# Optimization experiments

Hardware: AMD Instinct MI355X
Metric: run time of the kernel (lower is better)

## Reference

```python
import jax, jax.numpy as jnp
import numpy as np

N = 8192
NFEAT = 512
NHID = 512
NCLASS = 8
EPS = 1e-9
ADJ_P = 0.01  # edge density


def setup_inputs() -> dict:
    key = jax.random.key(0)
    ks = jax.random.split(key, 16)
    adj = (jax.random.uniform(ks[0], (N, N)) < ADJ_P).astype(jnp.float32)
    x = jax.random.normal(ks[1], (N, NFEAT), dtype=jnp.float32)
    s_in = 1.0 / np.sqrt(NFEAT)
    s_h = 1.0 / np.sqrt(NHID)
    return {
        "adj": adj,
        "x": x,
        "gcn1_W": jax.random.normal(ks[2], (NFEAT, NHID), jnp.float32) * s_in,
        "gcn1_b": jnp.zeros((NHID,), jnp.float32),
        "Qw": jax.random.normal(ks[3], (NHID, NHID), jnp.float32) * s_h,
        "Qb": jnp.zeros((NHID,), jnp.float32),
        "Kw": jax.random.normal(ks[4], (NHID, NHID), jnp.float32) * s_h,
        "Kb": jnp.zeros((NHID,), jnp.float32),
        "Vw": jax.random.normal(ks[5], (NHID, NHID), jnp.float32) * s_h,
        "Vb": jnp.zeros((NHID,), jnp.float32),
        "ln_g": jnp.ones((NHID,), jnp.float32),
        "ln_b": jnp.zeros((NHID,), jnp.float32),
        "gcn2_W": jax.random.normal(ks[6], (NHID, NCLASS), jnp.float32) * s_h,
        "gcn2_b": jnp.zeros((NCLASS,), jnp.float32),
    }


def _gcn_norm(a):
    # symmetric degree normalization D^{-1/2} A D^{-1/2}, degrees = row sums
    d_inv_sqrt = jax.lax.rsqrt(a.sum(axis=1) + EPS)  # [N]
    return d_inv_sqrt[:, None] * a * d_inv_sqrt[None, :]


def _layer_norm(x, g, b):
    mu = x.mean(axis=-1, keepdims=True)
    var = x.var(axis=-1, keepdims=True)
    return (x - mu) * jax.lax.rsqrt(var + 1e-5) * g + b


def reference(adj, x, gcn1_W, gcn1_b, Qw, Qb, Kw, Kb, Vw, Vb, ln_g, ln_b, gcn2_W, gcn2_b):
    # GraphConvolution: adj @ (x W) + b, then ReLU
    h = jax.nn.relu(adj @ (x @ gcn1_W) + gcn1_b)  # [N, NHID]
    Qh = h @ Qw + Qb
    Kh = h @ Kw + Kb
    Vh = h @ Vw + Vb
    # adjacency-masked dense scores (multiplicative mask, as in original)
    A_tilde = adj * (Qh @ Kh.T)  # [N, N]
    attention = jax.nn.softmax(A_tilde, axis=1)
    X_tilde = _gcn_norm(attention) @ Vh  # [N, NHID]
    X_tilde = _layer_norm(X_tilde, ln_g, ln_b)
    z = adj @ (X_tilde @ gcn2_W) + gcn2_b  # [N, NCLASS]
    return jax.nn.softmax(z, axis=1)
```

## Files before the change

kernel.cpp:

```cpp
#include <hip/hip_runtime.h>
#include <math.h>

#define N_NODES 8192
#define NFEAT 512
#define NHID 512
#define NCLASS 8
#define RCAP 192
#define KB_SPLIT 1536
#define KA_SPLIT 1024
#define CANDCAP 64
#define FILTER_MARGIN 96.0f
#define SROWS 4

#define PB_SPLITA 256
#define PB_SPLITB (PB_SPLITA + 4096)
#define PB_SPLITV (PB_SPLITB + 768)
#define PB_BIAS   (PB_SPLITV + 768)
#define PB_MISC   (PB_BIAS + 129)
#define PB_TOTAL  (PB_MISC + 6)

__device__ inline ushort f2bf(float f) {
  uint32_t u = __float_as_uint(f);
  uint32_t r = u + 0x7fffu + ((u >> 16) & 1u);
  return (ushort)(r >> 16);
}
__device__ inline float bf2f(ushort h) { return __uint_as_float(((uint32_t)h) << 16); }

__global__ __launch_bounds__(256) void build_ell(const float* __restrict__ adj,
                                                 int* __restrict__ colidx,
                                                 int* __restrict__ deg) {
  int row = blockIdx.x;
  __shared__ int cnt;
  __shared__ int cols[RCAP];
  if (threadIdx.x == 0) cnt = 0;
  __syncthreads();
  const float4* arow = (const float4*)(adj + (size_t)row * N_NODES);
#pragma unroll
  for (int it = 0; it < N_NODES / 4 / 256; ++it) {
    int i = it * 256 + threadIdx.x;
    float4 v = arow[i];
    int base = i * 4;
    if (v.x > 0.5f) { int p = atomicAdd(&cnt, 1); if (p < RCAP) cols[p] = base; }
    if (v.y > 0.5f) { int p = atomicAdd(&cnt, 1); if (p < RCAP) cols[p] = base + 1; }
    if (v.z > 0.5f) { int p = atomicAdd(&cnt, 1); if (p < RCAP) cols[p] = base + 2; }
    if (v.w > 0.5f) { int p = atomicAdd(&cnt, 1); if (p < RCAP) cols[p] = base + 3; }
    __syncthreads();
  }
  int d = cnt < RCAP ? cnt : RCAP;
  if (threadIdx.x == 0) deg[row] = d;
  for (int i = threadIdx.x; i < d; i += 256) colidx[(size_t)row * RCAP + i] = cols[i];
}

__global__ __launch_bounds__(256) void prep_all(
    const float* __restrict__ Kw, float* __restrict__ KwT,
    const float* __restrict__ x, ushort* __restrict__ Xs,
    const float* __restrict__ W1, ushort* __restrict__ W1ts,
    const float* __restrict__ Vw, ushort* __restrict__ Bcts,
    const float* __restrict__ Qw, const float* __restrict__ Qb, const float* __restrict__ Kb,
    float* __restrict__ u, float* __restrict__ w, float* __restrict__ cbuf,
    const float* __restrict__ Vb, float* __restrict__ bcat, float* __restrict__ T) {
  __shared__ float tile[32][33];
  int b = blockIdx.x, t = threadIdx.x;
  if (b < PB_SPLITA) {
    int bx = b & 15, by = b >> 4;
    int tx = t & 31, ty = t >> 5;
    int xcol = bx * 32 + tx, y0 = by * 32;
    for (int i = ty; i < 32; i += 8) tile[i][tx] = Kw[(size_t)(y0 + i) * 512 + xcol];
    __syncthreads();
    int xo = by * 32 + tx, yo0 = bx * 32;
    for (int i = ty; i < 32; i += 8) KwT[(size_t)(yo0 + i) * 512 + xo] = tile[tx][i];
  } else if (b < PB_SPLITB) {
    int idx = (b - PB_SPLITA) * 256 + t;
    int m = idx >> 7, tc = idx & 127;
    float4 v = ((const float4*)(x + (size_t)m * 512))[tc];
    ushort4 hi, lo;
    hi.x = f2bf(v.x); hi.y = f2bf(v.y); hi.z = f2bf(v.z); hi.w = f2bf(v.w);
    lo.x = f2bf(v.x - bf2f(hi.x)); lo.y = f2bf(v.y - bf2f(hi.y));
    lo.z = f2bf(v.z - bf2f(hi.z)); lo.w = f2bf(v.w - bf2f(hi.w));
    ushort* row = Xs + (size_t)m * KA_SPLIT;
    ((ushort4*)row)[tc] = hi;
    ((ushort4*)(row + 512))[tc] = lo;
  } else if (b < PB_SPLITV) {
    int idx = (b - PB_SPLITB) * 256 + t;
    int n = idx / 384, tc = idx % 384;
    int sec = tc >> 7;
    int k0 = (tc & 127) << 2;
    ushort4 o;
    float f0 = W1[(size_t)(k0 + 0) * 512 + n];
    float f1 = W1[(size_t)(k0 + 1) * 512 + n];
    float f2 = W1[(size_t)(k0 + 2) * 512 + n];
    float f3 = W1[(size_t)(k0 + 3) * 512 + n];
    if (sec == 1) {
      o.x = f2bf(f0 - bf2f(f2bf(f0))); o.y = f2bf(f1 - bf2f(f2bf(f1)));
      o.z = f2bf(f2 - bf2f(f2bf(f2))); o.w = f2bf(f3 - bf2f(f2bf(f3)));
    } else {
      o.x = f2bf(f0); o.y = f2bf(f1); o.z = f2bf(f2); o.w = f2bf(f3);
    }
    ((ushort4*)(W1ts + (size_t)n * KB_SPLIT))[tc] = o;
  } else if (b < PB_BIAS) {
    int idx = (b - PB_SPLITV) * 256 + t;
    int n = idx / 384, tc = idx % 384;
    const float* src = Vw + n;
    int sec = tc >> 7;
    int k0 = (tc & 127) << 2;
    ushort4 o;
    float f0 = src[(size_t)(k0 + 0) * 512];
    float f1 = src[(size_t)(k0 + 1) * 512];
    float f2 = src[(size_t)(k0 + 2) * 512];
    float f3 = src[(size_t)(k0 + 3) * 512];
    if (sec == 1) {
      o.x = f2bf(f0 - bf2f(f2bf(f0))); o.y = f2bf(f1 - bf2f(f2bf(f1)));
      o.z = f2bf(f2 - bf2f(f2bf(f2))); o.w = f2bf(f3 - bf2f(f2bf(f3)));
    } else {
      o.x = f2bf(f0); o.y = f2bf(f1); o.z = f2bf(f2); o.w = f2bf(f3);
    }
    ((ushort4*)(Bcts + (size_t)(512 + n) * KB_SPLIT))[tc] = o;
  } else if (b < PB_MISC) {
    int k = (b - PB_BIAS) * 4 + (t >> 6);
    int lane = t & 63;
    if (k > NHID) return;
    if (k == NHID) {
      float s = 0.f;
      for (int j = lane; j < NHID; j += 64) s = fmaf(Qb[j], Kb[j], s);
#pragma unroll
      for (int o = 32; o > 0; o >>= 1) s += __shfl_down(s, o, 64);
      if (lane == 0) cbuf[0] = s;
      return;
    }
    float su = 0.f, sw = 0.f;
    for (int j = lane; j < NHID; j += 64) {
      su = fmaf(Qw[(size_t)k * NHID + j], Kb[j], su);
      sw = fmaf(Kw[(size_t)k * NHID + j], Qb[j], sw);
    }
#pragma unroll
    for (int o = 32; o > 0; o >>= 1) { su += __shfl_down(su, o, 64); sw += __shfl_down(sw, o, 64); }
    if (lane == 0) { u[k] = su; w[k] = sw; }
  } else {
    int i = (b - PB_MISC) * 256 + t;
    if (i < 1024) bcat[i] = (i < 512) ? 0.f : Vb[i - 512];
    else if (i < 1536) T[i - 1024] = 0.f;
  }
}

__global__ __launch_bounds__(256) void split_mmat(const float* __restrict__ Mm, ushort* __restrict__ Bt) {
  int idx = blockIdx.x * 256 + threadIdx.x;
  int n = idx / 384, tc = idx % 384;
  const float* src = Mm + n;
  int sec = tc >> 7;
  int k0 = (tc & 127) << 2;
  ushort4 o;
  float f0 = src[(size_t)(k0 + 0) * 512];
  float f1 = src[(size_t)(k0 + 1) * 512];
  float f2 = src[(size_t)(k0 + 2) * 512];
  float f3 = src[(size_t)(k0 + 3) * 512];
  if (sec == 1) {
    o.x = f2bf(f0 - bf2f(f2bf(f0))); o.y = f2bf(f1 - bf2f(f2bf(f1)));
    o.z = f2bf(f2 - bf2f(f2bf(f2))); o.w = f2bf(f3 - bf2f(f2bf(f3)));
  } else {
    o.x = f2bf(f0); o.y = f2bf(f1); o.z = f2bf(f2); o.w = f2bf(f3);
  }
  ((ushort4*)(Bt + (size_t)n * KB_SPLIT))[tc] = o;
}

__global__ __launch_bounds__(256) void sgemm64x128(const float* __restrict__ A,
                                                   const float* __restrict__ B,
                                                   float* __restrict__ C,
                                                   int M, int Nn, int K, int ldc) {
  __shared__ float As[16][68];
  __shared__ float Bs[16][132];
  const int tid = threadIdx.x;
  const int bm = blockIdx.y * 64, bn = blockIdx.x * 128;
  const int tx = tid & 15, ty = tid >> 4;
  const int arow = tid >> 2, acol = (tid & 3) << 2;
  const int brow = tid >> 4, bcol = (tid & 15) << 2;
  float acc[4][8];
#pragma unroll
  for (int i = 0; i < 4; ++i)
#pragma unroll
    for (int j = 0; j < 8; ++j) acc[i][j] = 0.f;
  const float* Ap = A + (size_t)(bm + arow) * K + acol;
  const float* Bp = B + (size_t)brow * Nn + bn + bcol;
  float4 av = *(const float4*)(Ap);
  float4 bv0 = *(const float4*)(Bp);
  float4 bv1 = *(const float4*)(Bp + 64);
  for (int k0 = 0; k0 < K; k0 += 16) {
    if (k0) __syncthreads();
    As[acol + 0][arow] = av.x;
    As[acol + 1][arow] = av.y;
    As[acol + 2][arow] = av.z;
    As[acol + 3][arow] = av.w;
    *(float4*)&Bs[brow][bcol] = bv0;
    *(float4*)&Bs[brow][bcol + 64] = bv1;
    __syncthreads();
    int kn = (k0 + 16 < K) ? k0 + 16 : 0;
    av = *(const float4*)(Ap + kn);
    bv0 = *(const float4*)(Bp + (size_t)kn * Nn);
    bv1 = *(const float4*)(Bp + (size_t)kn * Nn + 64);
#pragma unroll
    for (int kk = 0; kk < 16; ++kk) {
      float4 a = *(const float4*)&As[kk][ty << 2];
      float4 b0 = *(const float4*)&Bs[kk][tx << 2];
      float4 b1 = *(const float4*)&Bs[kk][(tx << 2) + 64];
      float ar[4] = {a.x, a.y, a.z, a.w};
      float br[8] = {b0.x, b0.y, b0.z, b0.w, b1.x, b1.y, b1.z, b1.w};
#pragma unroll
      for (int i = 0; i < 4; ++i)
#pragma unroll
        for (int j = 0; j < 8; ++j) acc[i][j] = fmaf(ar[i], br[j], acc[i][j]);
    }
  }
#pragma unroll
  for (int i = 0; i < 4; ++i) {
    int r = bm + (ty << 2) + i;
    *(float4*)(C + (size_t)r * ldc + bn + (tx << 2)) =
        make_float4(acc[i][0], acc[i][1], acc[i][2], acc[i][3]);
    *(float4*)(C + (size_t)r * ldc + bn + 64 + (tx << 2)) =
        make_float4(acc[i][4], acc[i][5], acc[i][6], acc[i][7]);
  }
}

using frag_ab = __attribute__((ext_vector_type(8))) short;
using frag_cd = __attribute__((ext_vector_type(4))) float;

__global__ __launch_bounds__(256) void mfma_gemm_bt(const ushort* __restrict__ A,
                                                    const ushort* __restrict__ Bt,
                                                    const float* __restrict__ bias,
                                                    float* __restrict__ C,
                                                    int ldc, float* __restrict__ Tsum) {
  __shared__ __align__(16) ushort Atile[128 * 64];
  __shared__ __align__(16) ushort Btile[128 * 64];
  const int tid = threadIdx.x;
  const int w = tid >> 6, lane = tid & 63;
  const int m0 = blockIdx.y * 128, n0 = blockIdx.x * 128;
  const int wm = (w >> 1) * 64, wn = (w & 1) * 64;
  const int q = lane >> 4, c16 = lane & 15;

  frag_cd acc[4][4];
#pragma unroll
  for (int i = 0; i < 4; ++i)
#pragma unroll
    for (int j = 0; j < 4; ++j) acc[i][j] = (frag_cd){0.f, 0.f, 0.f, 0.f};

  const int srow = (w << 3) + (lane >> 3);
  const int scolb = (lane & 7) << 4;
  const uint8_t* gA = (const uint8_t*)A + (size_t)(m0 + srow) * (KA_SPLIT * 2) + scolb;
  const uint8_t* gB = (const uint8_t*)Bt + (size_t)(n0 + srow) * (KB_SPLIT * 2) + scolb;

  for (int c = 0; c < 24; ++c) {
    const size_t kaB = (size_t)((c < 8 ? c : c - 8) * 128);
    const size_t kbB = (size_t)(c * 128);
#pragma unroll
    for (int r = 0; r < 4; ++r) {
      __builtin_amdgcn_global_load_lds(
          (const __attribute__((address_space(1))) uint32_t*)(gA + (size_t)(r * 32) * (KA_SPLIT * 2) + kaB),
          (__attribute__((address_space(3))) uint32_t*)((uint8_t*)Atile + r * 4096 + w * 1024), 16, 0, 0);
      __builtin_amdgcn_global_load_lds(
          (const __attribute__((address_space(1))) uint32_t*)(gB + (size_t)(r * 32) * (KB_SPLIT * 2) + kbB),
          (__attribute__((address_space(3))) uint32_t*)((uint8_t*)Btile + r * 4096 + w * 1024), 16, 0, 0);
    }
    __syncthreads();
#pragma unroll
    for (int kk = 0; kk < 2; ++kk) {
      frag_ab af[4], bf[4];
#pragma unroll
      for (int i = 0; i < 4; ++i) {
        af[i] = *(const frag_ab*)((const uint8_t*)Atile + (wm + i * 16 + c16) * 128 + kk * 64 + q * 16);
        bf[i] = *(const frag_ab*)((const uint8_t*)Btile + (wn + i * 16 + c16) * 128 + kk * 64 + q * 16);
      }
#pragma unroll
      for (int i = 0; i < 4; ++i)
#pragma unroll
        for (int j = 0; j < 4; ++j)
          acc[i][j] = __builtin_amdgcn_mfma_f32_16x16x32_bf16(af[i], bf[j], acc[i][j], 0, 0, 0);
    }
    __syncthreads();
  }
#pragma unroll
  for (int j = 0; j < 4; ++j) {
    int col = n0 + wn + j * 16 + c16;
    float bv = bias ? bias[col] : 0.f;
    float csum = 0.f;
#pragma unroll
    for (int i = 0; i < 4; ++i) {
      int row = m0 + wm + i * 16 + q * 4;
#pragma unroll
      for (int r = 0; r < 4; ++r) {
        float v = acc[i][j][r] + bv;
        C[(size_t)(row + r) * ldc + col] = v;
        csum += v;
      }
    }
    if (Tsum && col >= 512) {
      csum += __shfl_xor(csum, 16, 64);
      csum += __shfl_xor(csum, 32, 64);
      if (q == 0) atomicAdd(&Tsum[col - 512], csum);
    }
  }
}

__global__ __launch_bounds__(256, 8) void spmm_persist(const float* __restrict__ xW,
                                                       const int* __restrict__ colidx,
                                                       const int* __restrict__ deg,
                                                       const float* __restrict__ b1,
                                                       const float* __restrict__ u, const float* __restrict__ w,
                                                       float* __restrict__ h, ushort* __restrict__ Hs,
                                                       float* __restrict__ a_vec, float* __restrict__ b_vec) {
  __shared__ int scols[SROWS][RCAP];
  __shared__ float4 part[128];
  __shared__ float ra[2], rb[2];
  int t = threadIdx.x, half = t >> 7, tt = t & 127;
  int row0 = blockIdx.x * SROWS;
  int d[SROWS];
#pragma unroll
  for (int r = 0; r < SROWS; ++r) {
    d[r] = deg[row0 + r];
    for (int i = t; i < d[r]; i += 256) scols[r][i] = colidx[(size_t)(row0 + r) * RCAP + i];
  }
  __syncthreads();
#pragma unroll 1
  for (int r = 0; r < SROWS; ++r) {
    int row = row0 + r, dd = d[r];
    float4 acc = make_float4(0.f, 0.f, 0.f, 0.f);
    int e = half;
    for (; e + 14 < dd; e += 16) {
      float4 v0 = ((const float4*)(xW + (size_t)scols[r][e + 0] * NHID))[tt];
      float4 v1 = ((const float4*)(xW + (size_t)scols[r][e + 2] * NHID))[tt];
      float4 v2 = ((const float4*)(xW + (size_t)scols[r][e + 4] * NHID))[tt];
      float4 v3 = ((const float4*)(xW + (size_t)scols[r][e + 6] * NHID))[tt];
      float4 v4 = ((const float4*)(xW + (size_t)scols[r][e + 8] * NHID))[tt];
      float4 v5 = ((const float4*)(xW + (size_t)scols[r][e + 10] * NHID))[tt];
      float4 v6 = ((const float4*)(xW + (size_t)scols[r][e + 12] * NHID))[tt];
      float4 v7 = ((const float4*)(xW + (size_t)scols[r][e + 14] * NHID))[tt];
      acc.x += ((v0.x + v1.x) + (v2.x + v3.x)) + ((v4.x + v5.x) + (v6.x + v7.x));
      acc.y += ((v0.y + v1.y) + (v2.y + v3.y)) + ((v4.y + v5.y) + (v6.y + v7.y));
      acc.z += ((v0.z + v1.z) + (v2.z + v3.z)) + ((v4.z + v5.z) + (v6.z + v7.z));
      acc.w += ((v0.w + v1.w) + (v2.w + v3.w)) + ((v4.w + v5.w) + (v6.w + v7.w));
    }
    for (; e < dd; e += 2) {
      float4 v = ((const float4*)(xW + (size_t)scols[r][e] * NHID))[tt];
      acc.x += v.x; acc.y += v.y; acc.z += v.z; acc.w += v.w;
    }
    if (half == 1) part[tt] = acc;
    __syncthreads();
    if (half == 0) {
      float4 p = part[tt];
      acc.x += p.x; acc.y += p.y; acc.z += p.z; acc.w += p.w;
      float4 bv = ((const float4*)b1)[tt];
      float4 o = make_float4(fmaxf(acc.x + bv.x, 0.f), fmaxf(acc.y + bv.y, 0.f),
                             fmaxf(acc.z + bv.z, 0.f), fmaxf(acc.w + bv.w, 0.f));
      ((float4*)(h + (size_t)row * NHID))[tt] = o;
      ushort4 hi, lo;
      hi.x = f2bf(o.x); hi.y = f2bf(o.y); hi.z = f2bf(o.z); hi.w = f2bf(o.w);
      lo.x = f2bf(o.x - bf2f(hi.x)); lo.y = f2bf(o.y - bf2f(hi.y));
      lo.z = f2bf(o.z - bf2f(hi.z)); lo.w = f2bf(o.w - bf2f(hi.w));
      ushort* hr = Hs + (size_t)row * KA_SPLIT;
      ((ushort4*)hr)[tt] = hi;
      ((ushort4*)(hr + 512))[tt] = lo;
      float4 uv = ((const float4*)u)[tt], wv4 = ((const float4*)w)[tt];
      float sa = fmaf(o.x, uv.x, fmaf(o.y, uv.y, fmaf(o.z, uv.z, o.w * uv.w)));
      float sb = fmaf(o.x, wv4.x, fmaf(o.y, wv4.y, fmaf(o.z, wv4.z, o.w * wv4.w)));
      int wid = tt >> 6, lane = tt & 63;
#pragma unroll
      for (int off = 32; off > 0; off >>= 1) { sa += __shfl_down(sa, off, 64); sb += __shfl_down(sb, off, 64); }
      if (lane == 0) { ra[wid] = sa; rb[wid] = sb; }
    }
    __syncthreads();
    if (t == 0) { a_vec[row] = ra[0] + ra[1]; b_vec[row] = rb[0] + rb[1]; }
    __syncthreads();
  }
}

__global__ __launch_bounds__(256) void score2_agg_ln(
    const float* __restrict__ G, int ldg, const float* __restrict__ h,
    const ushort* __restrict__ Hs, const int* __restrict__ colidx, const int* __restrict__ deg,
    const float* __restrict__ a_vec, const float* __restrict__ b_vec,
    const float* __restrict__ cbuf, const float* __restrict__ Vh, int ldv,
    const float* __restrict__ T, const float* __restrict__ lng,
    const float* __restrict__ lnb, const float* __restrict__ W2, float* __restrict__ Y) {
  __shared__ int scols[4][RCAP];
  __shared__ float sbv[4][RCAP];
  __shared__ float sv[4][RCAP];
  __shared__ int cand[4][CANDCAP];
  __shared__ int ccnt[4];
  __shared__ float w2s[NHID * NCLASS];
  int t = threadIdx.x, wv = t >> 6, lane = t & 63;
  int row = blockIdx.x * 4 + wv;
  int d = deg[row];
  int q = lane >> 4, u = lane & 15;
  for (int i = t; i < NHID * NCLASS; i += 256) w2s[i] = W2[i];
  if (lane == 0) ccnt[wv] = 0;
  float4 ga4[4][2];
  const float4* Gr4 = (const float4*)(G + (size_t)row * ldg);
#pragma unroll
  for (int it2 = 0; it2 < 4; ++it2) {
    ga4[it2][0] = Gr4[it2 * 32 + 2 * u];
    ga4[it2][1] = Gr4[it2 * 32 + 2 * u + 1];
  }
  for (int i = lane; i < d; i += 64) {
    int c = colidx[(size_t)row * RCAP + i];
    scols[wv][i] = c;
    sbv[wv][i] = b_vec[c];
  }
  __syncthreads();
  for (int e0 = 0; e0 < d; e0 += 4) {
    int e = e0 + q;
    bool act = e < d;
    int col = scols[wv][act ? e : 0];
    const uint4* hr = (const uint4*)(Hs + (size_t)col * KA_SPLIT);
    float s_a = 0.f, s_b = 0.f;
#pragma unroll
    for (int it2 = 0; it2 < 4; ++it2) {
      uint4 p = hr[it2 * 16 + u];
      float4 g0 = ga4[it2][0], g1 = ga4[it2][1];
      s_a = fmaf(__uint_as_float(p.x << 16), g0.x, s_a);
      s_a = fmaf(__uint_as_float(p.x & 0xffff0000u), g0.y, s_a);
      s_a = fmaf(__uint_as_float(p.y << 16), g0.z, s_a);
      s_a = fmaf(__uint_as_float(p.y & 0xffff0000u), g0.w, s_a);
      s_b = fmaf(__uint_as_float(p.z << 16), g1.x, s_b);
      s_b = fmaf(__uint_as_float(p.z & 0xffff0000u), g1.y, s_b);
      s_b = fmaf(__uint_as_float(p.w << 16), g1.z, s_b);
      s_b = fmaf(__uint_as_float(p.w & 0xffff0000u), g1.w, s_b);
    }
    float s = s_a + s_b;
    s += __shfl_down(s, 8, 16);
    s += __shfl_down(s, 4, 16);
    s += __shfl_down(s, 2, 16);
    s += __shfl_down(s, 1, 16);
    if (u == 0 && act) sv[wv][e] = s + sbv[wv][e];
  }
  __syncthreads();
  float fm = -1e30f;
  for (int i = lane; i < d; i += 64) fm = fmaxf(fm, sv[wv][i]);
#pragma unroll
  for (int o = 32; o > 0; o >>= 1) fm = fmaxf(fm, __shfl_xor(fm, o, 64));
  for (int i = lane; i < d; i += 64) {
    if (sv[wv][i] >= fm - FILTER_MARGIN) {
      int p = atomicAdd(&ccnt[wv], 1);
      if (p < CANDCAP) cand[wv][p] = i;
    }
  }
  __syncthreads();
  int nc = ccnt[wv];
  bool ovf = nc > CANDCAP;
  if (ovf) nc = d;
  float ai = a_vec[row] + cbuf[0];
  for (int c0 = 0; c0 < nc; c0 += 4) {
    int idx = c0 + q;
    bool act = idx < nc;
    int e = act ? (ovf ? idx : cand[wv][idx]) : 0;
    int col = scols[wv][e];
    const float4* hr = (const float4*)(h + (size_t)col * NHID);
    float s_a = 0.f, s_b = 0.f;
#pragma unroll
    for (int it2 = 0; it2 < 4; ++it2) {
      float4 h0 = hr[it2 * 32 + 2 * u], h1 = hr[it2 * 32 + 2 * u + 1];
      float4 g0 = ga4[it2][0], g1 = ga4[it2][1];
      s_a = fmaf(h0.x, g0.x, s_a); s_a = fmaf(h0.y, g0.y, s_a);
      s_a = fmaf(h0.z, g0.z, s_a); s_a = fmaf(h0.w, g0.w, s_a);
      s_b = fmaf(h1.x, g1.x, s_b); s_b = fmaf(h1.y, g1.y, s_b);
      s_b = fmaf(h1.z, g1.z, s_b); s_b = fmaf(h1.w, g1.w, s_b);
    }
    float s = s_a + s_b;
    s += __shfl_down(s, 8, 16);
    s += __shfl_down(s, 4, 16);
    s += __shfl_down(s, 2, 16);
    s += __shfl_down(s, 1, 16);
    if (u == 0 && act) sv[wv][e] = s + ai + sbv[wv][e];
  }
  __syncthreads();
  float m = 0.f;
  for (int i = lane; i < nc; i += 64) {
    int e = ovf ? i : cand[wv][i];
    m = fmaxf(m, sv[wv][e]);
  }
#pragma unroll
  for (int o = 32; o > 0; o >>= 1) m = fmaxf(m, __shfl_xor(m, o, 64));
  float ssum = 0.f;
  for (int i = lane; i < nc; i += 64) {
    int e = ovf ? i : cand[wv][i];
    float ex = expf(sv[wv][e] - m);
    sv[wv][e] = ex;
    ssum += ex;
  }
#pragma unroll
  for (int o = 32; o > 0; o >>= 1) ssum += __shfl_xor(ssum, o, 64);
  float em = expf(-m);
  float inv = 1.f / (ssum + (float)(N_NODES - d) * em);
  float ci = em * inv;
  __syncthreads();
  float4 a0 = make_float4(0.f, 0.f, 0.f, 0.f), a1 = a0;
  for (int i = 0; i < nc; ++i) {
    int e = ovf ? i : cand[wv][i];
    float we = sv[wv][e] * inv;
    if (we > 1e-12f) {
      const float4* vr = (const float4*)(Vh + (size_t)scols[wv][e] * ldv);
      float4 v0 = vr[lane * 2], v1 = vr[lane * 2 + 1];
      a0.x = fmaf(we, v0.x, a0.x); a0.y = fmaf(we, v0.y, a0.y);
      a0.z = fmaf(we, v0.z, a0.z); a0.w = fmaf(we, v0.w, a0.w);
      a1.x = fmaf(we, v1.x, a1.x); a1.y = fmaf(we, v1.y, a1.y);
      a1.z = fmaf(we, v1.z, a1.z); a1.w = fmaf(we, v1.w, a1.w);
    }
  }
  float4 t0 = ((const float4*)T)[lane * 2], t1 = ((const float4*)T)[lane * 2 + 1];
  a0.x = fmaf(ci, t0.x, a0.x); a0.y = fmaf(ci, t0.y, a0.y);
  a0.z = fmaf(ci, t0.z, a0.z); a0.w = fmaf(ci, t0.w, a0.w);
  a1.x = fmaf(ci, t1.x, a1.x); a1.y = fmaf(ci, t1.y, a1.y);
  a1.z = fmaf(ci, t1.z, a1.z); a1.w = fmaf(ci, t1.w, a1.w);
  float s1 = ((a0.x + a0.y) + (a0.z + a0.w)) + ((a1.x + a1.y) + (a1.z + a1.w));
  float s2 = ((a0.x * a0.x + a0.y * a0.y) + (a0.z * a0.z + a0.w * a0.w)) +
             ((a1.x * a1.x + a1.y * a1.y) + (a1.z * a1.z + a1.w * a1.w));
#pragma unroll
  for (int o = 32; o > 0; o >>= 1) { s1 += __shfl_xor(s1, o, 64); s2 += __shfl_xor(s2, o, 64); }
  float mu = s1 * (1.f / NHID);
  float var = s2 * (1.f / NHID) - mu * mu;
  float rstd = rsqrtf(var + 1e-5f);
  float4 g0 = ((const float4*)lng)[lane * 2], g1 = ((const float4*)lng)[lane * 2 + 1];
  float4 b0 = ((const float4*)lnb)[lane * 2], b1v = ((const float4*)lnb)[lane * 2 + 1];
  float4 o0, o1;
  o0.x = (a0.x - mu) * rstd * g0.x + b0.x;
  o0.y = (a0.y - mu) * rstd * g0.y + b0.y;
  o0.z = (a0.z - mu) * rstd * g0.z + b0.z;
  o0.w = (a0.w - mu) * rstd * g0.w + b0.w;
  o1.x = (a1.x - mu) * rstd * g1.x + b1v.x;
  o1.y = (a1.y - mu) * rstd * g1.y + b1v.y;
  o1.z = (a1.z - mu) * rstd * g1.z + b1v.z;
  o1.w = (a1.w - mu) * rstd * g1.w + b1v.w;
  float xv[8] = {o0.x, o0.y, o0.z, o0.w, o1.x, o1.y, o1.z, o1.w};
  float accc[NCLASS];
#pragma unroll
  for (int c = 0; c < NCLASS; ++c) accc[c] = 0.f;
#pragma unroll
  for (int kk = 0; kk < 8; ++kk) {
    int k = lane * 8 + kk;
#pragma unroll
    for (int c = 0; c < NCLASS; ++c) accc[c] = fmaf(xv[kk], w2s[k * NCLASS + c], accc[c]);
  }
#pragma unroll
  for (int c = 0; c < NCLASS; ++c)
#pragma unroll
    for (int o = 32; o > 0; o >>= 1) accc[c] += __shfl_down(accc[c], o, 64);
  if (lane == 0) {
    *(float4*)(Y + (size_t)row * NCLASS) = make_float4(accc[0], accc[1], accc[2], accc[3]);
    *(float4*)(Y + (size_t)row * NCLASS + 4) = make_float4(accc[4], accc[5], accc[6], accc[7]);
  }
}

__global__ __launch_bounds__(256) void final_spmm_softmax(const float* __restrict__ Y,
                                                          const int* __restrict__ colidx,
                                                          const int* __restrict__ deg,
                                                          const float* __restrict__ b2,
                                                          float* __restrict__ out) {
  int t = threadIdx.x;
  int wv = t >> 6, lane = t & 63;
  int row = blockIdx.x * 4 + wv;
  int d = deg[row];
  const int* cols = colidx + (size_t)row * RCAP;
  float acc[8];
#pragma unroll
  for (int c = 0; c < 8; ++c) acc[c] = 0.f;
  for (int e = lane; e < d; e += 64) {
    int col = cols[e];
    const float4* yr = (const float4*)(Y + (size_t)col * 8);
    float4 y0 = yr[0], y1 = yr[1];
    acc[0] += y0.x; acc[1] += y0.y; acc[2] += y0.z; acc[3] += y0.w;
    acc[4] += y1.x; acc[5] += y1.y; acc[6] += y1.z; acc[7] += y1.w;
  }
#pragma unroll
  for (int c = 0; c < 8; ++c)
#pragma unroll
    for (int o = 32; o > 0; o >>= 1) acc[c] += __shfl_down(acc[c], o, 64);
  if (lane == 0) {
    float z[8];
    float m = -1e30f;
#pragma unroll
    for (int c = 0; c < 8; ++c) { z[c] = acc[c] + b2[c]; m = fmaxf(m, z[c]); }
    float s = 0.f;
#pragma unroll
    for (int c = 0; c < 8; ++c) { z[c] = expf(z[c] - m); s += z[c]; }
    float inv = 1.f / s;
    *(float4*)(out + (size_t)row * 8) = make_float4(z[0] * inv, z[1] * inv, z[2] * inv, z[3] * inv);
    *(float4*)(out + (size_t)row * 8 + 4) = make_float4(z[4] * inv, z[5] * inv, z[6] * inv, z[7] * inv);
  }
}

extern "C" void kernel_launch(void* const* d_in, const int* in_sizes, int n_in,
                              void* d_out, int out_size, void* d_ws, size_t ws_size,
                              hipStream_t stream) {
  const float* adj = (const float*)d_in[0];
  const float* x = (const float*)d_in[1];
  const float* W1 = (const float*)d_in[2];
  const float* b1 = (const float*)d_in[3];
  const float* Qw = (const float*)d_in[4];
  const float* Qb = (const float*)d_in[5];
  const float* Kw = (const float*)d_in[6];
  const float* Kb = (const float*)d_in[7];
  const float* Vw = (const float*)d_in[8];
  const float* Vb = (const float*)d_in[9];
  const float* ln_g = (const float*)d_in[10];
  const float* ln_b = (const float*)d_in[11];
  const float* W2 = (const float*)d_in[12];
  const float* b2 = (const float*)d_in[13];
  float* out = (float*)d_out;

  char* ws = (char*)d_ws;
  size_t off = 0;
  auto alloc = [&](size_t bytes) -> void* {
    void* p = ws + off;
    off = (off + bytes + 255) & ~(size_t)255;
    return p;
  };
  int* colidx = (int*)alloc((size_t)N_NODES * RCAP * 4);
  int* deg = (int*)alloc((size_t)N_NODES * 4);
  float* bufA = (float*)alloc((size_t)N_NODES * NHID * 4);
  float* bufB = (float*)alloc((size_t)N_NODES * NHID * 4);
  float* GVh = (float*)alloc((size_t)N_NODES * 1024 * 4);
  ushort* Xs = (ushort*)alloc((size_t)N_NODES * KA_SPLIT * 2);
  ushort* Hs = (ushort*)alloc((size_t)N_NODES * KA_SPLIT * 2);
  ushort* W1ts = (ushort*)alloc((size_t)512 * KB_SPLIT * 2);
  ushort* Bcts = (ushort*)alloc((size_t)1024 * KB_SPLIT * 2);
  float* KwT = (float*)alloc((size_t)512 * 512 * 4);
  float* Mmat = (float*)alloc((size_t)512 * 512 * 4);
  float* bcat = (float*)alloc((size_t)1024 * 4);
  float* a_vec = (float*)alloc((size_t)N_NODES * 4);
  float* b_vec = (float*)alloc((size_t)N_NODES * 4);
  float* u_vec = (float*)alloc((size_t)NHID * 4);
  float* w_vec = (float*)alloc((size_t)NHID * 4);
  float* cbuf = (float*)alloc(256);
  float* T = (float*)alloc((size_t)NHID * 4);
  float* Y = (float*)alloc((size_t)N_NODES * NCLASS * 4);
  (void)in_sizes; (void)n_in; (void)out_size; (void)ws_size;

  build_ell<<<N_NODES, 256, 0, stream>>>(adj, colidx, deg);
  prep_all<<<PB_TOTAL, 256, 0, stream>>>(Kw, KwT, x, Xs, W1, W1ts, Vw, Bcts,
                                         Qw, Qb, Kb, u_vec, w_vec, cbuf, Vb, bcat, T);
  sgemm64x128<<<dim3(4, 8), 256, 0, stream>>>(Qw, KwT, Mmat, 512, 512, 512, 512);
  mfma_gemm_bt<<<dim3(4, 64), 256, 0, stream>>>(Xs, W1ts, nullptr, bufA, 512, nullptr);
  split_mmat<<<(512 * 384) / 256, 256, 0, stream>>>(Mmat, Bcts);
  spmm_persist<<<N_NODES / SROWS, 256, 0, stream>>>(bufA, colidx, deg, b1, u_vec, w_vec,
                                                    bufB, Hs, a_vec, b_vec);
  mfma_gemm_bt<<<dim3(8, 64), 256, 0, stream>>>(Hs, Bcts, bcat, GVh, 1024, T);
  score2_agg_ln<<<N_NODES / 4, 256, 0, stream>>>(GVh, 1024, bufB, Hs, colidx, deg, a_vec, b_vec,
                                                 cbuf, GVh + 512, 1024, T, ln_g, ln_b, W2, Y);
  final_spmm_softmax<<<N_NODES / 4, 256, 0, stream>>>(Y, colidx, deg, b2, out);
}
```

Measured before the change: 757.0 us.

## Merge independent kernels into combined launches to cut launch count

Measured after the change: 723.7 us. 4.4% less time.

```diff
diff --git a/kernel.cpp b/kernel.cpp
--- a/kernel.cpp
+++ b/kernel.cpp
@@ -26,32 +26,8 @@
 }
 __device__ inline float bf2f(ushort h) { return __uint_as_float(((uint32_t)h) << 16); }
 
-__global__ __launch_bounds__(256) void build_ell(const float* __restrict__ adj,
-                                                 int* __restrict__ colidx,
-                                                 int* __restrict__ deg) {
-  int row = blockIdx.x;
-  __shared__ int cnt;
-  __shared__ int cols[RCAP];
-  if (threadIdx.x == 0) cnt = 0;
-  __syncthreads();
-  const float4* arow = (const float4*)(adj + (size_t)row * N_NODES);
-#pragma unroll
-  for (int it = 0; it < N_NODES / 4 / 256; ++it) {
-    int i = it * 256 + threadIdx.x;
-    float4 v = arow[i];
-    int base = i * 4;
-    if (v.x > 0.5f) { int p = atomicAdd(&cnt, 1); if (p < RCAP) cols[p] = base; }
-    if (v.y > 0.5f) { int p = atomicAdd(&cnt, 1); if (p < RCAP) cols[p] = base + 1; }
-    if (v.z > 0.5f) { int p = atomicAdd(&cnt, 1); if (p < RCAP) cols[p] = base + 2; }
-    if (v.w > 0.5f) { int p = atomicAdd(&cnt, 1); if (p < RCAP) cols[p] = base + 3; }
-    __syncthreads();
-  }
-  int d = cnt < RCAP ? cnt : RCAP;
-  if (threadIdx.x == 0) deg[row] = d;
-  for (int i = threadIdx.x; i < d; i += 256) colidx[(size_t)row * RCAP + i] = cols[i];
-}
-
-__global__ __launch_bounds__(256) void prep_all(
+__global__ __launch_bounds__(256) void build_prep(
+    const float* __restrict__ adj, int* __restrict__ colidx, int* __restrict__ deg,
     const float* __restrict__ Kw, float* __restrict__ KwT,
     const float* __restrict__ x, ushort* __restrict__ Xs,
     const float* __restrict__ W1, ushort* __restrict__ W1ts,
@@ -59,8 +35,32 @@
     const float* __restrict__ Qw, const float* __restrict__ Qb, const float* __restrict__ Kb,
     float* __restrict__ u, float* __restrict__ w, float* __restrict__ cbuf,
     const float* __restrict__ Vb, float* __restrict__ bcat, float* __restrict__ T) {
+  __shared__ int cnt;
+  __shared__ int cols[RCAP];
   __shared__ float tile[32][33];
-  int b = blockIdx.x, t = threadIdx.x;
+  int bid = blockIdx.x, t = threadIdx.x;
+  if (bid < N_NODES) {
+    int row = bid;
+    if (t == 0) cnt = 0;
+    __syncthreads();
+    const float4* arow = (const float4*)(adj + (size_t)row * N_NODES);
+#pragma unroll
+    for (int it = 0; it < N_NODES / 4 / 256; ++it) {
+      int i = it * 256 + t;
+      float4 v = arow[i];
+      int base = i * 4;
+      if (v.x > 0.5f) { int p = atomicAdd(&cnt, 1); if (p < RCAP) cols[p] = base; }
+      if (v.y > 0.5f) { int p = atomicAdd(&cnt, 1); if (p < RCAP) cols[p] = base + 1; }
+      if (v.z > 0.5f) { int p = atomicAdd(&cnt, 1); if (p < RCAP) cols[p] = base + 2; }
+      if (v.w > 0.5f) { int p = atomicAdd(&cnt, 1); if (p < RCAP) cols[p] = base + 3; }
+      __syncthreads();
+    }
+    int d = cnt < RCAP ? cnt : RCAP;
+    if (t == 0) deg[row] = d;
+    for (int i = t; i < d; i += 256) colidx[(size_t)row * RCAP + i] = cols[i];
+    return;
+  }
+  int b = bid - N_NODES;
   if (b < PB_SPLITA) {
     int bx = b & 15, by = b >> 4;
     int tx = t & 31, ty = t >> 5;
@@ -142,34 +142,89 @@
   }
 }
 
-__global__ __launch_bounds__(256) void split_mmat(const float* __restrict__ Mm, ushort* __restrict__ Bt) {
-  int idx = blockIdx.x * 256 + threadIdx.x;
-  int n = idx / 384, tc = idx % 384;
-  const float* src = Mm + n;
-  int sec = tc >> 7;
-  int k0 = (tc & 127) << 2;
-  ushort4 o;
-  float f0 = src[(size_t)(k0 + 0) * 512];
-  float f1 = src[(size_t)(k0 + 1) * 512];
-  float f2 = src[(size_t)(k0 + 2) * 512];
-  float f3 = src[(size_t)(k0 + 3) * 512];
-  if (sec == 1) {
-    o.x = f2bf(f0 - bf2f(f2bf(f0))); o.y = f2bf(f1 - bf2f(f2bf(f1)));
-    o.z = f2bf(f2 - bf2f(f2bf(f2))); o.w = f2bf(f3 - bf2f(f2bf(f3)));
-  } else {
-    o.x = f2bf(f0); o.y = f2bf(f1); o.z = f2bf(f2); o.w = f2bf(f3);
-  }
-  ((ushort4*)(Bt + (size_t)n * KB_SPLIT))[tc] = o;
-}
-
-__global__ __launch_bounds__(256) void sgemm64x128(const float* __restrict__ A,
-                                                   const float* __restrict__ B,
-                                                   float* __restrict__ C,
-                                                   int M, int Nn, int K, int ldc) {
-  __shared__ float As[16][68];
-  __shared__ float Bs[16][132];
+using frag_ab = __attribute__((ext_vector_type(8))) short;
+using frag_cd = __attribute__((ext_vector_type(4))) float;
+
+__device__ void mfma_gemm_body(int bx, int by, const ushort* __restrict__ A,
+                               const ushort* __restrict__ Bt, const float* __restrict__ bias,
+                               float* __restrict__ C, int ldc, float* __restrict__ Tsum,
+                               ushort* Atile, ushort* Btile) {
   const int tid = threadIdx.x;
-  const int bm = blockIdx.y * 64, bn = blockIdx.x * 128;
+  const int w = tid >> 6, lane = tid & 63;
+  const int m0 = by * 128, n0 = bx * 128;
+  const int wm = (w >> 1) * 64, wn = (w & 1) * 64;
+  const int q = lane >> 4, c16 = lane & 15;
+
+  frag_cd acc[4][4];
+#pragma unroll
+  for (int i = 0; i < 4; ++i)
+#pragma unroll
+    for (int j = 0; j < 4; ++j) acc[i][j] = (frag_cd){0.f, 0.f, 0.f, 0.f};
+
+  const int srow = (w << 3) + (lane >> 3);
+  const int scolb = (lane & 7) << 4;
+  const uint8_t* gA = (const uint8_t*)A + (size_t)(m0 + srow) * (KA_SPLIT * 2) + scolb;
+  const uint8_t* gB = (const uint8_t*)Bt + (size_t)(n0 + srow) * (KB_SPLIT * 2) + scolb;
+
+  for (int c = 0; c < 24; ++c) {
+    const size_t kaB = (size_t)((c < 8 ? c : c - 8) * 128);
+    const size_t kbB = (size_t)(c * 128);
+#pragma unroll
+    for (int r = 0; r < 4; ++r) {
+      __builtin_amdgcn_global_load_lds(
+          (const __attribute__((address_space(1))) uint32_t*)(gA + (size_t)(r * 32) * (KA_SPLIT * 2) + kaB),
+          (__attribute__((address_space(3))) uint32_t*)((uint8_t*)Atile + r * 4096 + w * 1024), 16, 0, 0);
+      __builtin_amdgcn_global_load_lds(
+          (const __attribute__((address_space(1))) uint32_t*)(gB + (size_t)(r * 32) * (KB_SPLIT * 2) + kbB),
+          (__attribute__((address_space(3))) uint32_t*)((uint8_t*)Btile + r * 4096 + w * 1024), 16, 0, 0);
+    }
+    __syncthreads();
+#pragma unroll
+    for (int kk = 0; kk < 2; ++kk) {
+      frag_ab af[4], bf[4];
+#pragma unroll
+      for (int i = 0; i < 4; ++i) {
+        af[i] = *(const frag_ab*)((const uint8_t*)Atile + (wm + i * 16 + c16) * 128 + kk * 64 + q * 16);
+        bf[i] = *(const frag_ab*)((const uint8_t*)Btile + (wn + i * 16 + c16) * 128 + kk * 64 + q * 16);
+      }
+#pragma unroll
+      for (int i = 0; i < 4; ++i)
+#pragma unroll
+        for (int j = 0; j < 4; ++j)
+          acc[i][j] = __builtin_amdgcn_mfma_f32_16x16x32_bf16(af[i], bf[j], acc[i][j], 0, 0, 0);
+    }
+    __syncthreads();
+  }
+#pragma unroll
+  for (int j = 0; j < 4; ++j) {
+    int col = n0 + wn + j * 16 + c16;
+    float bv = bias ? bias[col] : 0.f;
+    float csum = 0.f;
+#pragma unroll
+    for (int i = 0; i < 4; ++i) {
+      int row = m0 + wm + i * 16 + q * 4;
+#pragma unroll
+      for (int r = 0; r < 4; ++r) {
+        float v = acc[i][j][r] + bv;
+        C[(size_t)(row + r) * ldc + col] = v;
+        csum += v;
+      }
+    }
+    if (Tsum && col >= 512) {
+      csum += __shfl_xor(csum, 16, 64);
+      csum += __shfl_xor(csum, 32, 64);
+      if (q == 0) atomicAdd(&Tsum[col - 512], csum);
+    }
+  }
+}
+
+__device__ void sgemm_body(int bx, int by, const float* __restrict__ A, const float* __restrict__ B,
+                           float* __restrict__ C, char* smem) {
+  float(*As)[68] = (float(*)[68])smem;
+  float(*Bs)[132] = (float(*)[132])(smem + 16 * 68 * 4);
+  const int M = 512, Nn = 512, K = 512, ldc = 512;
+  const int tid = threadIdx.x;
+  const int bm = by * 64, bn = bx * 128;
   const int tx = tid & 15, ty = tid >> 4;
   const int arow = tid >> 2, acol = (tid & 3) << 2;
   const int brow = tid >> 4, bcol = (tid & 15) << 2;
@@ -217,98 +272,62 @@
     *(float4*)(C + (size_t)r * ldc + bn + 64 + (tx << 2)) =
         make_float4(acc[i][4], acc[i][5], acc[i][6], acc[i][7]);
   }
-}
-
-using frag_ab = __attribute__((ext_vector_type(8))) short;
-using frag_cd = __attribute__((ext_vector_type(4))) float;
-
-__global__ __launch_bounds__(256) void mfma_gemm_bt(const ushort* __restrict__ A,
-                                                    const ushort* __restrict__ Bt,
-                                                    const float* __restrict__ bias,
-                                                    float* __restrict__ C,
-                                                    int ldc, float* __restrict__ Tsum) {
+  (void)M;
+}
+
+__global__ __launch_bounds__(256) void gemm1_sgemm(
+    const ushort* __restrict__ Xs, const ushort* __restrict__ W1ts, float* __restrict__ xW,
+    const float* __restrict__ Qw, const float* __restrict__ KwT, float* __restrict__ Mmat) {
+  __shared__ __align__(16) char smem[32768];
+  int b = blockIdx.x;
+  if (b < 256) {
+    mfma_gemm_body(b & 3, b >> 2, Xs, W1ts, nullptr, xW, 512, nullptr,
+                   (ushort*)smem, (ushort*)(smem + 16384));
+  } else {
+    sgemm_body((b - 256) & 3, (b - 256) >> 2, Qw, KwT, Mmat, smem);
+  }
+}
+
+__global__ __launch_bounds__(256) void mfma_gemm2(const ushort* __restrict__ Hs,
+                                                  const ushort* __restrict__ Bcts,
+                                                  const float* __restrict__ bcat,
+                                                  float* __restrict__ GVh, float* __restrict__ T) {
   __shared__ __align__(16) ushort Atile[128 * 64];
   __shared__ __align__(16) ushort Btile[128 * 64];
-  const int tid = threadIdx.x;
-  const int w = tid >> 6, lane = tid & 63;
-  const int m0 = blockIdx.y * 128, n0 = blockIdx.x * 128;
-  const int wm = (w >> 1) * 64, wn = (w & 1) * 64;
-  const int q = lane >> 4, c16 = lane & 15;
-
-  frag_cd acc[4][4];
-#pragma unroll
-  for (int i = 0; i < 4; ++i)
-#pragma unroll
-    for (int j = 0; j < 4; ++j) acc[i][j] = (frag_cd){0.f, 0.f, 0.f, 0.f};
-
-  const int srow = (w << 3) + (lane >> 3);
-  const int scolb = (lane & 7) << 4;
-  const uint8_t* gA = (const uint8_t*)A + (size_t)(m0 + srow) * (KA_SPLIT * 2) + scolb;
-  const uint8_t* gB = (const uint8_t*)Bt + (size_t)(n0 + srow) * (KB_SPLIT * 2) + scolb;
-
-  for (int c = 0; c < 24; ++c) {
-    const size_t kaB = (size_t)((c < 8 ? c : c - 8) * 128);
-    const size_t kbB = (size_t)(c * 128);
-#pragma unroll
-    for (int r = 0; r < 4; ++r) {
-      __builtin_amdgcn_global_load_lds(
-          (const __attribute__((address_space(1))) uint32_t*)(gA + (size_t)(r * 32) * (KA_SPLIT * 2) + kaB),
-          (__attribute__((address_space(3))) uint32_t*)((uint8_t*)Atile + r * 4096 + w * 1024), 16, 0, 0);
-      __builtin_amdgcn_global_load_lds(
-          (const __attribute__((address_space(1))) uint32_t*)(gB + (size_t)(r * 32) * (KB_SPLIT * 2) + kbB),
-          (__attribute__((address_space(3))) uint32_t*)((uint8_t*)Btile + r * 4096 + w * 1024), 16, 0, 0);
-    }
-    __syncthreads();
-#pragma unroll
-    for (int kk = 0; kk < 2; ++kk) {
-      frag_ab af[4], bf[4];
-#pragma unroll
-      for (int i = 0; i < 4; ++i) {
-        af[i] = *(const frag_ab*)((const uint8_t*)Atile + (wm + i * 16 + c16) * 128 + kk * 64 + q * 16);
-        bf[i] = *(const frag_ab*)((const uint8_t*)Btile + (wn + i * 16 + c16) * 128 + kk * 64 + q * 16);
-      }
-#pragma unroll
-      for (int i = 0; i < 4; ++i)
-#pragma unroll
-        for (int j = 0; j < 4; ++j)
-          acc[i][j] = __builtin_amdgcn_mfma_f32_16x16x32_bf16(af[i], bf[j], acc[i][j], 0, 0, 0);
-    }
-    __syncthreads();
-  }
-#pragma unroll
-  for (int j = 0; j < 4; ++j) {
-    int col = n0 + wn + j * 16 + c16;
-    float bv = bias ? bias[col] : 0.f;
-    float csum = 0.f;
-#pragma unroll
-    for (int i = 0; i < 4; ++i) {
-      int row = m0 + wm + i * 16 + q * 4;
-#pragma unroll
-      for (int r = 0; r < 4; ++r) {
-        float v = acc[i][j][r] + bv;
-        C[(size_t)(row + r) * ldc + col] = v;
-        csum += v;
-      }
-    }
-    if (Tsum && col >= 512) {
-      csum += __shfl_xor(csum, 16, 64);
-      csum += __shfl_xor(csum, 32, 64);
-      if (q == 0) atomicAdd(&Tsum[col - 512], csum);
-    }
-  }
-}
-
-__global__ __launch_bounds__(256, 8) void spmm_persist(const float* __restrict__ xW,
-                                                       const int* __restrict__ colidx,
-                                                       const int* __restrict__ deg,
-                                                       const float* __restrict__ b1,
-                                                       const float* __restrict__ u, const float* __restrict__ w,
-                                                       float* __restrict__ h, ushort* __restrict__ Hs,
-                                                       float* __restrict__ a_vec, float* __restrict__ b_vec) {
+  mfma_gemm_body(blockIdx.x, blockIdx.y, Hs, Bcts, bcat, GVh, 1024, T, Atile, Btile);
+}
+
+__global__ __launch_bounds__(256, 8) void spmm_split(
+    const float* __restrict__ xW, const int* __restrict__ colidx, const int* __restrict__ deg,
+    const float* __restrict__ b1, const float* __restrict__ u, const float* __restrict__ w,
+    float* __restrict__ h, ushort* __restrict__ Hs,
+    float* __restrict__ a_vec, float* __restrict__ b_vec,
+    const float* __restrict__ Mm, ushort* __restrict__ Bt) {
   __shared__ int scols[SROWS][RCAP];
   __shared__ float4 part[128];
   __shared__ float ra[2], rb[2];
-  int t = threadIdx.x, half = t >> 7, tt = t & 127;
+  int t = threadIdx.x;
+  if (blockIdx.x >= N_NODES / SROWS) {
+    int idx = (blockIdx.x - N_NODES / SROWS) * 256 + t;
+    int n = idx / 384, tc = idx % 384;
+    const float* src = Mm + n;
+    int sec = tc >> 7;
+    int k0 = (tc & 127) << 2;
+    ushort4 o;
+    float f0 = src[(size_t)(k0 + 0) * 512];
+    float f1 = src[(size_t)(k0 + 1) * 512];
+    float f2 = src[(size_t)(k0 + 2) * 512];
+    float f3 = src[(size_t)(k0 + 3) * 512];
+    if (sec == 1) {
+      o.x = f2bf(f0 - bf2f(f2bf(f0))); o.y = f2bf(f1 - bf2f(f2bf(f1)));
+      o.z = f2bf(f2 - bf2f(f2bf(f2))); o.w = f2bf(f3 - bf2f(f2bf(f3)));
+    } else {
+      o.x = f2bf(f0); o.y = f2bf(f1); o.z = f2bf(f2); o.w = f2bf(f3);
+    }
+    ((ushort4*)(Bt + (size_t)n * KB_SPLIT))[tc] = o;
+    return;
+  }
+  int half = t >> 7, tt = t & 127;
   int row0 = blockIdx.x * SROWS;
   int d[SROWS];
 #pragma unroll
@@ -630,15 +649,13 @@
   float* Y = (float*)alloc((size_t)N_NODES * NCLASS * 4);
   (void)in_sizes; (void)n_in; (void)out_size; (void)ws_size;
 
-  build_ell<<<N_NODES, 256, 0, stream>>>(adj, colidx, deg);
-  prep_all<<<PB_TOTAL, 256, 0, stream>>>(Kw, KwT, x, Xs, W1, W1ts, Vw, Bcts,
-                                         Qw, Qb, Kb, u_vec, w_vec, cbuf, Vb, bcat, T);
-  sgemm64x128<<<dim3(4, 8), 256, 0, stream>>>(Qw, KwT, Mmat, 512, 512, 512, 512);
-  mfma_gemm_bt<<<dim3(4, 64), 256, 0, stream>>>(Xs, W1ts, nullptr, bufA, 512, nullptr);
-  split_mmat<<<(512 * 384) / 256, 256, 0, stream>>>(Mmat, Bcts);
-  spmm_persist<<<N_NODES / SROWS, 256, 0, stream>>>(bufA, colidx, deg, b1, u_vec, w_vec,
-                                                    bufB, Hs, a_vec, b_vec);
-  mfma_gemm_bt<<<dim3(8, 64), 256, 0, stream>>>(Hs, Bcts, bcat, GVh, 1024, T);
+  build_prep<<<N_NODES + PB_TOTAL, 256, 0, stream>>>(
+      adj, colidx, deg, Kw, KwT, x, Xs, W1, W1ts, Vw, Bcts,
+      Qw, Qb, Kb, u_vec, w_vec, cbuf, Vb, bcat, T);
+  gemm1_sgemm<<<256 + 32, 256, 0, stream>>>(Xs, W1ts, bufA, Qw, KwT, Mmat);
+  spmm_split<<<N_NODES / SROWS + 768, 256, 0, stream>>>(
+      bufA, colidx, deg, b1, u_vec, w_vec, bufB, Hs, a_vec, b_vec, Mmat, Bcts);
+  mfma_gemm2<<<dim3(8, 64), 256, 0, stream>>>(Hs, Bcts, bcat, GVh, T);
   score2_agg_ln<<<N_NODES / 4, 256, 0, stream>>>(GVh, 1024, bufB, Hs, colidx, deg, a_vec, b_vec,
                                                  cbuf, GVh + 512, 1024, T, ln_g, ln_b, W2, Y);
   final_spmm_softmax<<<N_NODES / 4, 256, 0, stream>>>(Y, colidx, deg, b2, out);
```
